# Optimization experiments

Measured on AMD Instinct MI355X. Metric: run time of the kernel, lower is better.

Reference implementation:

```python
import jax, jax.numpy as jnp
import numpy as np

D_MODEL = 2048
N_HEADS = 16
HEAD_DIM = D_MODEL // N_HEADS  # 128
HIDDEN = int(8 * D_MODEL / 3)  # 5461
EPS = 1e-6


def setup_inputs() -> dict:
    key = jax.random.key(0)
    ks = jax.random.split(key, 12)
    B, S = 2, 2048
    std = D_MODEL ** -0.5
    return {
        "x": jax.random.normal(ks[0], (B, S, D_MODEL), jnp.float32),
        "freq_cis": jax.random.normal(ks[1], (S, HEAD_DIM // 2, 2, 2), jnp.float32),
        "wq": jax.random.normal(ks[2], (D_MODEL, D_MODEL), jnp.float32) * std,
        "wk": jax.random.normal(ks[3], (D_MODEL, D_MODEL), jnp.float32) * std,
        "wv": jax.random.normal(ks[4], (D_MODEL, D_MODEL), jnp.float32) * std,
        "wo": jax.random.normal(ks[5], (D_MODEL, D_MODEL), jnp.float32) * std,
        "bo": jnp.zeros((D_MODEL,), jnp.float32),
        "w1": jax.random.normal(ks[6], (HIDDEN, D_MODEL), jnp.float32) * std,
        "w3": jax.random.normal(ks[7], (HIDDEN, D_MODEL), jnp.float32) * std,
        "w2": jax.random.normal(ks[8], (D_MODEL, HIDDEN), jnp.float32) * (HIDDEN ** -0.5),
        "g_attn": jnp.ones((D_MODEL,), jnp.float32),
        "g_ffn": jnp.ones((D_MODEL,), jnp.float32),
    }


def rmsnorm(x, g):
    xf = x.astype(jnp.float32)
    return xf * jax.lax.rsqrt(jnp.mean(xf * xf, axis=-1, keepdims=True) + EPS) * g


def rope(xq, xk, f):
    # xq/xk: [b, s, h, hd]; f: [s, hd/2, 2, 2]
    b, s, h, hd = xq.shape
    xq_ = xq.reshape(b, s, h, hd // 2, 2)
    xk_ = xk.reshape(b, s, h, hd // 2, 2)
    # out[b,s,h,i,j] = sum_k x[b,s,h,i,k] * f[s,i,j,k]
    q = jnp.einsum("bshik,sijk->bshij", xq_, f).reshape(b, s, h, hd)
    k = jnp.einsum("bshik,sijk->bshij", xk_, f).reshape(b, s, h, hd)
    return q, k


def reference(x, freq_cis, wq, wk, wv, wo, bo, w1, w3, w2, g_attn, g_ffn):
    b, s, d = x.shape
    h, hd = N_HEADS, HEAD_DIM
    scale = hd ** -0.5

    # --- attention sublayer ---
    xn = rmsnorm(x, g_attn)
    q = jnp.einsum("bsd,ed->bse", xn, wq).reshape(b, s, h, hd)
    k = jnp.einsum("bsd,ed->bse", xn, wk).reshape(b, s, h, hd)
    v = jnp.einsum("bsd,ed->bse", xn, wv).reshape(b, s, h, hd)
    q, k = rope(q, k, freq_cis[:s])
    attn = jnp.einsum("bqhd,bkhd->bhqk", q, k) * scale
    attn = jax.nn.softmax(attn, axis=-1)
    o = jnp.einsum("bhqk,bkhd->bqhd", attn, v).reshape(b, s, d)
    o = jnp.einsum("bsd,ed->bse", o, wo) + bo
    hres = x + o

    # --- SwiGLU FFN sublayer ---
    hn = rmsnorm(hres, g_ffn)
    x1 = jnp.einsum("bsd,hd->bsh", hn, w1)
    x3 = jnp.einsum("bsd,hd->bsh", hn, w3)
    ffn = jnp.einsum("bsh,dh->bsd", jax.nn.silu(x1) * x3, w2)
    return hres + ffn
```

## Files before the change

### kernel.cpp

```cpp
#include <hip/hip_runtime.h>

#define D_MODEL 2048
#define NHEADS 16
#define HDIM 128
#define HIDDEN_ 5461
#define HP2 5632
#define BATCH 2
#define SEQ 2048
#define MTOK 4096

typedef unsigned short u16;
typedef __attribute__((ext_vector_type(8))) short bf16x8;
typedef __attribute__((ext_vector_type(4))) float f32x4;

__device__ __forceinline__ u16 f2b(float f) {
  union { float f; unsigned u; } v; v.f = f;
  return (u16)((v.u + 0x7FFFu + ((v.u >> 16) & 1u)) >> 16);
}
__device__ __forceinline__ float b2f(u16 u) {
  union { unsigned u; float f; } v; v.u = ((unsigned)u) << 16;
  return v.f;
}
__device__ __forceinline__ void gload16(const void* g, void* l) {
  __builtin_amdgcn_global_load_lds(
      (const __attribute__((address_space(1))) unsigned int*)g,
      (__attribute__((address_space(3))) unsigned int*)l, 16, 0, 0);
}

#define SB0() __builtin_amdgcn_sched_barrier(0)
#define BARRIER() do { SB0(); __builtin_amdgcn_s_barrier(); SB0(); } while (0)
#define LGKM0() do { asm volatile("s_waitcnt lgkmcnt(0)" ::: "memory"); SB0(); } while (0)

__global__ __launch_bounds__(256) void k_conv8(const float* __restrict__ src,
                                               u16* __restrict__ dst, int n8) {
  int stride = gridDim.x * 256;
  for (int i = blockIdx.x * 256 + threadIdx.x; i < n8; i += stride) {
    const float4* s = (const float4*)src + (size_t)i * 2;
    float4 a = s[0], b = s[1];
    bf16x8 o;
    o[0] = f2b(a.x); o[1] = f2b(a.y); o[2] = f2b(a.z); o[3] = f2b(a.w);
    o[4] = f2b(b.x); o[5] = f2b(b.y); o[6] = f2b(b.z); o[7] = f2b(b.w);
    ((bf16x8*)dst)[i] = o;
  }
}

__global__ __launch_bounds__(256) void k_convpad(const float* __restrict__ src,
                                                 u16* __restrict__ dst,
                                                 int srows, int scols, int drows, int dcols) {
  size_t n = (size_t)drows * dcols;
  size_t stride = (size_t)gridDim.x * 256;
  for (size_t i = blockIdx.x * 256 + threadIdx.x; i < n; i += stride) {
    int r = (int)(i / dcols), c = (int)(i % dcols);
    float v = (r < srows && c < scols) ? src[(size_t)r * scols + c] : 0.f;
    dst[i] = f2b(v);
  }
}

__global__ __launch_bounds__(256) void k_rmsnorm(const float* __restrict__ X,
                                                 const float* __restrict__ G,
                                                 u16* __restrict__ Out) {
  int row = blockIdx.x;
  int tid = threadIdx.x;
  const float4* x4 = (const float4*)(X + (size_t)row * D_MODEL);
  float4 a = x4[tid * 2], b = x4[tid * 2 + 1];
  float ss = a.x * a.x + a.y * a.y + a.z * a.z + a.w * a.w +
             b.x * b.x + b.y * b.y + b.z * b.z + b.w * b.w;
#pragma unroll
  for (int off = 1; off < 64; off <<= 1) ss += __shfl_xor(ss, off);
  __shared__ float part[4];
  if ((tid & 63) == 0) part[tid >> 6] = ss;
  __syncthreads();
  float rstd = rsqrtf((part[0] + part[1] + part[2] + part[3]) * (1.0f / D_MODEL) + 1e-6f);
  const float4* g4 = (const float4*)G;
  float4 ga = g4[tid * 2], gb = g4[tid * 2 + 1];
  bf16x8 o;
  o[0] = f2b(a.x * rstd * ga.x); o[1] = f2b(a.y * rstd * ga.y);
  o[2] = f2b(a.z * rstd * ga.z); o[3] = f2b(a.w * rstd * ga.w);
  o[4] = f2b(b.x * rstd * gb.x); o[5] = f2b(b.y * rstd * gb.y);
  o[6] = f2b(b.z * rstd * gb.z); o[7] = f2b(b.w * rstd * gb.w);
  *((bf16x8*)(Out + (size_t)row * D_MODEL) + tid) = o;
}

template <int WN, int EPI>
__global__ __launch_bounds__(512, 2) void k_gemm2(const u16* __restrict__ A,
                                                  const u16* __restrict__ Bw,
                                                  void* __restrict__ O0,
                                                  void* __restrict__ O1,
                                                  void* __restrict__ O2,
                                                  const float* __restrict__ bias,
                                                  const float* __restrict__ res,
                                                  const u16* __restrict__ aux,
                                                  int M, int N, int K) {
  constexpr int BN = WN * 64;
  constexpr int PB = BN * 64;
  __shared__ __align__(128) char lds[65536 + 4 * PB];
  const int tid = threadIdx.x;
  const int w = tid >> 6, lane = tid & 63;
  const int lo = lane & 15, hi = lane >> 4;
  const int wr = w >> 2, wc = w & 3;

  const int ntN = N / BN;
  const int nwg = gridDim.x * gridDim.y;
  const int flat = blockIdx.y * gridDim.x + blockIdx.x;
  const int swz = (flat & 7) * (nwg >> 3) + (flat >> 3);
  const int tm = swz / ntN, tn = swz % ntN;
  const int m0 = tm * 256, n0 = tn * BN;

  auto stA = [&](int nb, int kk, int k0) {
#pragma unroll
    for (int j = 0; j < 2; ++j) {
      int row = j * 128 + (tid >> 2);
      const u16* g = A + (size_t)(m0 + row) * K + k0 + kk * 32 + (tid & 3) * 8;
      gload16(g, lds + nb * 32768 + kk * 16384 + j * 8192 + tid * 16);
    }
  };
  auto stB = [&](int nb, int kk, int k0) {
#pragma unroll
    for (int j = 0; j < WN / 2; ++j) {
      int row = j * 128 + (tid >> 2);
      const u16* g = Bw + (size_t)(n0 + row) * K + k0 + kk * 32 + (tid & 3) * 8;
      gload16(g, lds + 65536 + nb * 2 * PB + kk * PB + j * 8192 + tid * 16);
    }
  };
  auto ldA = [&](int buf, int kk, int mf) {
    return *(const bf16x8*)(lds + buf * 32768 + kk * 16384 +
                            (wr * 128 + mf * 16 + lo) * 64 + hi * 16);
  };
  auto ldB = [&](int buf, int kk, int nf) {
    return *(const bf16x8*)(lds + 65536 + buf * 2 * PB + kk * PB +
                            (wc * (WN * 16) + nf * 16 + lo) * 64 + hi * 16);
  };
#define VMCNT_CONFIRM()                                             \
  do {                                                              \
    if constexpr (WN == 4)                                          \
      asm volatile("s_waitcnt vmcnt(4)" ::: "memory");              \
    else                                                            \
      asm volatile("s_waitcnt vmcnt(3)" ::: "memory");              \
    SB0();                                                          \
  } while (0)

  f32x4 acc[8][WN];
#pragma unroll
  for (int i = 0; i < 8; i++)
#pragma unroll
    for (int j = 0; j < WN; j++) acc[i][j] = (f32x4){0.f, 0.f, 0.f, 0.f};

  stA(0, 0, 0);
  stB(0, 0, 0);
  stA(0, 1, 0);
  stB(0, 1, 0);
  VMCNT_CONFIRM();
  BARRIER();

  const int KT = K / 64;
  for (int kt = 0; kt < KT; ++kt) {
    const int buf = kt & 1, nb = buf ^ 1;
    int kn = (kt + 1) * 64;
    if (kn >= K) kn = 0;
    bf16x8 aF[4], bF[WN];

#pragma unroll
    for (int i = 0; i < 4; i++) aF[i] = ldA(buf, 0, i);
#pragma unroll
    for (int j = 0; j < WN; j++) bF[j] = ldB(buf, 0, j);
    stA(nb, 0, kn);
    BARRIER();
    LGKM0();
    __builtin_amdgcn_s_setprio(1);
#pragma unroll
    for (int i = 0; i < 4; i++)
#pragma unroll
      for (int j = 0; j < WN; j++)
        acc[i][j] = __builtin_amdgcn_mfma_f32_16x16x32_bf16(aF[i], bF[j], acc[i][j], 0, 0, 0);
    __builtin_amdgcn_s_setprio(0);
    BARRIER();

#pragma unroll
    for (int i = 0; i < 4; i++) aF[i] = ldA(buf, 0, 4 + i);
    stB(nb, 0, kn);
    VMCNT_CONFIRM();
    BARRIER();
    LGKM0();
    __builtin_amdgcn_s_setprio(1);
#pragma unroll
    for (int i = 0; i < 4; i++)
#pragma unroll
      for (int j = 0; j < WN; j++)
        acc[4 + i][j] = __builtin_amdgcn_mfma_f32_16x16x32_bf16(aF[i], bF[j], acc[4 + i][j], 0, 0, 0);
    __builtin_amdgcn_s_setprio(0);
    BARRIER();

#pragma unroll
    for (int i = 0; i < 4; i++) aF[i] = ldA(buf, 1, i);
#pragma unroll
    for (int j = 0; j < WN; j++) bF[j] = ldB(buf, 1, j);
    stA(nb, 1, kn);
    BARRIER();
    LGKM0();
    __builtin_amdgcn_s_setprio(1);
#pragma unroll
    for (int i = 0; i < 4; i++)
#pragma unroll
      for (int j = 0; j < WN; j++)
        acc[i][j] = __builtin_amdgcn_mfma_f32_16x16x32_bf16(aF[i], bF[j], acc[i][j], 0, 0, 0);
    __builtin_amdgcn_s_setprio(0);
    BARRIER();

#pragma unroll
    for (int i = 0; i < 4; i++) aF[i] = ldA(buf, 1, 4 + i);
    stB(nb, 1, kn);
    VMCNT_CONFIRM();
    BARRIER();
    LGKM0();
    __builtin_amdgcn_s_setprio(1);
#pragma unroll
    for (int i = 0; i < 4; i++)
#pragma unroll
      for (int j = 0; j < WN; j++)
        acc[4 + i][j] = __builtin_amdgcn_mfma_f32_16x16x32_bf16(aF[i], bF[j], acc[4 + i][j], 0, 0, 0);
    __builtin_amdgcn_s_setprio(0);
    BARRIER();
  }

  u16* qkvout = nullptr;
  int c0 = 0;
  if (EPI == 1) {
    int seg = n0 >> 11;
    qkvout = (u16*)(seg == 0 ? O0 : (seg == 1 ? O1 : O2));
    c0 = n0 & 2047;
  }
#pragma unroll
  for (int i = 0; i < 8; i++) {
#pragma unroll
    for (int j = 0; j < WN; j++) {
      int colL = wc * (WN * 16) + j * 16 + lo;
#pragma unroll
      for (int r = 0; r < 4; r++) {
        int row = m0 + wr * 128 + i * 16 + hi * 4 + r;
        float v = acc[i][j][r];
        if (EPI == 0) {
          ((u16*)O0)[(size_t)row * N + n0 + colL] = f2b(v);
        } else if (EPI == 1) {
          qkvout[(size_t)row * 2048 + c0 + colL] = f2b(v);
        } else if (EPI == 2) {
          size_t idx = (size_t)row * N + n0 + colL;
          ((float*)O0)[idx] = v + bias[n0 + colL] + res[idx];
        } else if (EPI == 3) {
          size_t idx = (size_t)row * N + n0 + colL;
          ((float*)O0)[idx] = v + res[idx];
        } else {
          size_t idx = (size_t)row * N + n0 + colL;
          float v1 = b2f(aux[idx]);
          float sig = 1.f / (1.f + __expf(-v1));
          ((u16*)O0)[idx] = f2b(v1 * sig * v);
        }
      }
    }
  }
#undef VMCNT_CONFIRM
}

__global__ __launch_bounds__(256) void k_rope(u16* __restrict__ Qb, u16* __restrict__ Kb,
                                              const float* __restrict__ F) {
  int n = MTOK * (D_MODEL / 2);
  int stride = gridDim.x * 256;
  for (int t = blockIdx.x * 256 + threadIdx.x; t < n; t += stride) {
    int i = t & 63;
    int rest = t >> 6;
    int hh = rest & 15;
    int tok = rest >> 4;
    int s = tok & (SEQ - 1);
    float4 f = ((const float4*)F)[s * 64 + i];
    size_t off = (size_t)tok * D_MODEL + hh * HDIM + i * 2;
    float x0 = b2f(Qb[off]), x1 = b2f(Qb[off + 1]);
    Qb[off] = f2b(x0 * f.x + x1 * f.y);
    Qb[off + 1] = f2b(x0 * f.z + x1 * f.w);
    x0 = b2f(Kb[off]); x1 = b2f(Kb[off + 1]);
    Kb[off] = f2b(x0 * f.x + x1 * f.y);
    Kb[off + 1] = f2b(x0 * f.z + x1 * f.w);
  }
}

__global__ __launch_bounds__(256) void k_vt(const u16* __restrict__ V, u16* __restrict__ VT) {
  __shared__ u16 t[64][72];
  const int stile = blockIdx.x;
  const int bh = blockIdx.y;
  const int dz = blockIdx.z;
  const int b = bh >> 4, h = bh & 15;
  const int tok0 = b * SEQ + stile * 64;
  const int d0 = dz * 64;
  const int tid = threadIdx.x;
#pragma unroll
  for (int p = 0; p < 2; p++) {
    int idx = p * 256 + tid;
    int row = idx >> 3, seg = idx & 7;
    bf16x8 v = *(const bf16x8*)(V + (size_t)(tok0 + row) * D_MODEL + h * HDIM + d0 + seg * 8);
    *(bf16x8*)(&t[row][seg * 8]) = v;
  }
  __syncthreads();
#pragma unroll
  for (int p = 0; p < 2; p++) {
    int idx = p * 256 + tid;
    int dr = idx >> 3, seg = idx & 7;
    bf16x8 o;
#pragma unroll
    for (int e = 0; e < 8; e++) o[e] = t[seg * 8 + e][dr];
    *(bf16x8*)(VT + ((size_t)bh * HDIM + d0 + dr) * SEQ + stile * 64 + seg * 8) = o;
  }
}

__global__ __launch_bounds__(256) void k_flash2(const u16* __restrict__ Q,
                                                const u16* __restrict__ Kb,
                                                const u16* __restrict__ VT,
                                                u16* __restrict__ O) {
  __shared__ u16 Kt[64 * 128];
  __shared__ u16 Vt[128 * 64];
  __shared__ u16 Pl[4][16 * 72];
  const int tid = threadIdx.x;
  const int w = tid >> 6, lane = tid & 63;
  const int lo = lane & 15, hi = lane >> 4;
  const int qt = blockIdx.x, bh = blockIdx.y;
  const int b = bh >> 4, h = bh & 15;
  const size_t qrow0 = (size_t)b * SEQ + qt * 64 + w * 16;
  const float SC = 0.08838834764831845f * 1.4426950408889634f;

  bf16x8 aQ[4];
#pragma unroll
  for (int kb = 0; kb < 4; kb++)
    aQ[kb] = *(const bf16x8*)(Q + (qrow0 + lo) * D_MODEL + h * HDIM + kb * 32 + hi * 8);

  float m_s[4], l_s[4];
  f32x4 oacc[8];
#pragma unroll
  for (int r = 0; r < 4; r++) { m_s[r] = -3.0e38f; l_s[r] = 0.f; }
#pragma unroll
  for (int d = 0; d < 8; d++) oacc[d] = (f32x4){0.f, 0.f, 0.f, 0.f};

  const int krowL = tid >> 4;
  const int kslot = (tid & 15) ^ (krowL & 7);
  const int vrowL = tid >> 3;
  const int vslot = (tid & 7) ^ (vrowL & 7);
  const u16* Kbase = Kb + (size_t)b * SEQ * D_MODEL + h * HDIM;
  const u16* Vbase = VT + (size_t)bh * HDIM * SEQ;

  for (int kt = 0; kt < SEQ / 64; kt++) {
    __syncthreads();
#pragma unroll
    for (int t = 0; t < 4; t++) {
      int row = t * 16 + krowL;
      const u16* g = Kbase + (size_t)(kt * 64 + row) * D_MODEL + kslot * 8;
      gload16(g, (char*)Kt + t * 4096 + tid * 16);
    }
#pragma unroll
    for (int t = 0; t < 4; t++) {
      int row = t * 32 + vrowL;
      const u16* g = Vbase + (size_t)row * SEQ + kt * 64 + vslot * 8;
      gload16(g, (char*)Vt + t * 4096 + tid * 16);
    }
    __syncthreads();

    f32x4 sf[4];
#pragma unroll
    for (int cb = 0; cb < 4; cb++) {
      f32x4 s = (f32x4){0.f, 0.f, 0.f, 0.f};
#pragma unroll
      for (int kb = 0; kb < 4; kb++) {
        int row = cb * 16 + lo;
        int ps = (kb * 4 + hi) ^ (lo & 7);
        bf16x8 bk = *(const bf16x8*)(Kt + row * 128 + ps * 8);
        s = __builtin_amdgcn_mfma_f32_16x16x32_bf16(aQ[kb], bk, s, 0, 0, 0);
      }
      sf[cb] = s;
    }

    float tm[4];
    bool okl = true;
#pragma unroll
    for (int r = 0; r < 4; r++) {
      float s0 = sf[0][r] * SC, s1 = sf[1][r] * SC;
      float s2 = sf[2][r] * SC, s3 = sf[3][r] * SC;
      sf[0][r] = s0; sf[1][r] = s1; sf[2][r] = s2; sf[3][r] = s3;
      float t = fmaxf(fmaxf(s0, s1), fmaxf(s2, s3));
#pragma unroll
      for (int off = 1; off < 16; off <<= 1) t = fmaxf(t, __shfl_xor(t, off));
      tm[r] = t;
      okl = okl && (t - m_s[r] <= 11.5f);
    }
    if (__all(okl)) {
#pragma unroll
      for (int r = 0; r < 4; r++) {
        float p0 = exp2f(sf[0][r] - m_s[r]), p1 = exp2f(sf[1][r] - m_s[r]);
        float p2 = exp2f(sf[2][r] - m_s[r]), p3 = exp2f(sf[3][r] - m_s[r]);
        float rs = (p0 + p1) + (p2 + p3);
#pragma unroll
        for (int off = 1; off < 16; off <<= 1) rs += __shfl_xor(rs, off);
        l_s[r] += rs;
        int prow = hi * 4 + r;
        Pl[w][prow * 72 + lo] = f2b(p0);
        Pl[w][prow * 72 + 16 + lo] = f2b(p1);
        Pl[w][prow * 72 + 32 + lo] = f2b(p2);
        Pl[w][prow * 72 + 48 + lo] = f2b(p3);
      }
    } else {
#pragma unroll
      for (int r = 0; r < 4; r++) {
        float mnew = fmaxf(m_s[r], tm[r]);
        float alpha = exp2f(m_s[r] - mnew);
        float p0 = exp2f(sf[0][r] - mnew), p1 = exp2f(sf[1][r] - mnew);
        float p2 = exp2f(sf[2][r] - mnew), p3 = exp2f(sf[3][r] - mnew);
        float rs = (p0 + p1) + (p2 + p3);
#pragma unroll
        for (int off = 1; off < 16; off <<= 1) rs += __shfl_xor(rs, off);
        l_s[r] = l_s[r] * alpha + rs;
        m_s[r] = mnew;
#pragma unroll
        for (int d = 0; d < 8; d++) oacc[d][r] *= alpha;
        int prow = hi * 4 + r;
        Pl[w][prow * 72 + lo] = f2b(p0);
        Pl[w][prow * 72 + 16 + lo] = f2b(p1);
        Pl[w][prow * 72 + 32 + lo] = f2b(p2);
        Pl[w][prow * 72 + 48 + lo] = f2b(p3);
      }
    }
    asm volatile("s_waitcnt lgkmcnt(0)" ::: "memory");
    bf16x8 aP[2];
#pragma unroll
    for (int ks = 0; ks < 2; ks++)
      aP[ks] = *(const bf16x8*)(&Pl[w][lo * 72 + ks * 32 + hi * 8]);
#pragma unroll
    for (int db = 0; db < 8; db++) {
#pragma unroll
      for (int ks = 0; ks < 2; ks++) {
        int row = db * 16 + lo;
        int ps = (ks * 4 + hi) ^ (lo & 7);
        bf16x8 bv = *(const bf16x8*)(Vt + row * 64 + ps * 8);
        oacc[db] = __builtin_amdgcn_mfma_f32_16x16x32_bf16(aP[ks], bv, oacc[db], 0, 0, 0);
      }
    }
  }
#pragma unroll
  for (int db = 0; db < 8; db++) {
#pragma unroll
    for (int r = 0; r < 4; r++) {
      size_t row = qrow0 + hi * 4 + r;
      float inv = 1.f / l_s[r];
      O[row * D_MODEL + h * HDIM + db * 16 + lo] = f2b(oacc[db][r] * inv);
    }
  }
}

extern "C" void kernel_launch(void* const* d_in, const int* in_sizes, int n_in,
                              void* d_out, int out_size, void* d_ws, size_t ws_size,
                              hipStream_t stream) {
  (void)in_sizes; (void)n_in; (void)out_size; (void)ws_size;
  const float* x  = (const float*)d_in[0];
  const float* fc = (const float*)d_in[1];
  const float* wq = (const float*)d_in[2];
  const float* wk = (const float*)d_in[3];
  const float* wv = (const float*)d_in[4];
  const float* wo = (const float*)d_in[5];
  const float* bo = (const float*)d_in[6];
  const float* w1 = (const float*)d_in[7];
  const float* w3 = (const float*)d_in[8];
  const float* w2 = (const float*)d_in[9];
  const float* ga = (const float*)d_in[10];
  const float* gf = (const float*)d_in[11];
  float* out = (float*)d_out;

  char* p = (char*)d_ws;
  auto alloc = [&](size_t bytes) { char* r = p; p += (bytes + 255) & ~(size_t)255; return r; };
  u16* xn  = (u16*)alloc((size_t)MTOK * D_MODEL * 2);
  u16* qb  = (u16*)alloc((size_t)MTOK * D_MODEL * 2);
  u16* kb  = (u16*)alloc((size_t)MTOK * D_MODEL * 2);
  u16* vb  = (u16*)alloc((size_t)MTOK * D_MODEL * 2);
  u16* x1  = (u16*)alloc((size_t)MTOK * HP2 * 2);
  u16* wsl = (u16*)alloc((size_t)3 * D_MODEL * D_MODEL * 2);
  u16* vbt = xn;
  u16* ob  = vb;
  u16* hn  = qb;

  k_rmsnorm<<<MTOK, 256, 0, stream>>>(x, ga, xn);
  k_conv8<<<1024, 256, 0, stream>>>(wq, wsl, D_MODEL * D_MODEL / 8);
  k_conv8<<<1024, 256, 0, stream>>>(wk, wsl + (size_t)D_MODEL * D_MODEL, D_MODEL * D_MODEL / 8);
  k_conv8<<<1024, 256, 0, stream>>>(wv, wsl + (size_t)2 * D_MODEL * D_MODEL, D_MODEL * D_MODEL / 8);
  k_gemm2<4, 1><<<dim3(6144 / 256, MTOK / 256), 512, 0, stream>>>(
      xn, wsl, qb, kb, vb, nullptr, nullptr, nullptr, MTOK, 6144, D_MODEL);
  k_rope<<<1024, 256, 0, stream>>>(qb, kb, fc);
  k_vt<<<dim3(SEQ / 64, BATCH * NHEADS, 2), 256, 0, stream>>>(vb, vbt);
  dim3 gfl(SEQ / 64, BATCH * NHEADS);
  k_flash2<<<gfl, 256, 0, stream>>>(qb, kb, vbt, ob);
  k_conv8<<<1024, 256, 0, stream>>>(wo, wsl, D_MODEL * D_MODEL / 8);
  k_gemm2<2, 2><<<dim3(2048 / 128, MTOK / 256), 512, 0, stream>>>(
      ob, wsl, out, nullptr, nullptr, bo, x, nullptr, MTOK, D_MODEL, D_MODEL);

  k_rmsnorm<<<MTOK, 256, 0, stream>>>(out, gf, hn);
  k_convpad<<<1024, 256, 0, stream>>>(w1, wsl, HIDDEN_, D_MODEL, HP2, D_MODEL);
  k_gemm2<4, 0><<<dim3(HP2 / 256, MTOK / 256), 512, 0, stream>>>(
      hn, wsl, x1, nullptr, nullptr, nullptr, nullptr, nullptr, MTOK, HP2, D_MODEL);
  k_convpad<<<1024, 256, 0, stream>>>(w3, wsl, HIDDEN_, D_MODEL, HP2, D_MODEL);
  k_gemm2<4, 4><<<dim3(HP2 / 256, MTOK / 256), 512, 0, stream>>>(
      hn, wsl, x1, nullptr, nullptr, nullptr, nullptr, x1, MTOK, HP2, D_MODEL);
  k_convpad<<<1024, 256, 0, stream>>>(w2, wsl, D_MODEL, HIDDEN_, D_MODEL, HP2);
  k_gemm2<2, 3><<<dim3(2048 / 128, MTOK / 256), 512, 0, stream>>>(
      x1, wsl, out, nullptr, nullptr, nullptr, out, nullptr, MTOK, D_MODEL, HP2);
}
```

Baseline: 852.8 us.

## Process two query tiles per wave in flash attention and retune GEMM tiles

The flash attention kernel now handles 128 query rows per block, two 16-row groups per wave. Each K and V fragment read from LDS is reused across both groups, and the MFMA operands are swapped to a transposed S/O layout. Softmax takes one max per column group with a packed bf16 convert, and the output store is vectorized. The three QKV weight conversions are merged into one launch, and several GEMMs switch to a narrower 128-column tile template. The cost is higher register pressure from doubled accumulators and more GEMM blocks.

Measured after the change: 819.3 us. 1.04x faster.

```diff
diff --git a/kernel.cpp b/kernel.cpp
--- a/kernel.cpp
+++ b/kernel.cpp
@@ -12,6 +12,7 @@
 typedef unsigned short u16;
 typedef __attribute__((ext_vector_type(8))) short bf16x8;
 typedef __attribute__((ext_vector_type(4))) float f32x4;
+typedef __attribute__((ext_vector_type(4))) short s16x4;
 
 __device__ __forceinline__ u16 f2b(float f) {
   union { float f; unsigned u; } v; v.f = f;
@@ -37,6 +38,25 @@
   for (int i = blockIdx.x * 256 + threadIdx.x; i < n8; i += stride) {
     const float4* s = (const float4*)src + (size_t)i * 2;
     float4 a = s[0], b = s[1];
+    bf16x8 o;
+    o[0] = f2b(a.x); o[1] = f2b(a.y); o[2] = f2b(a.z); o[3] = f2b(a.w);
+    o[4] = f2b(b.x); o[5] = f2b(b.y); o[6] = f2b(b.z); o[7] = f2b(b.w);
+    ((bf16x8*)dst)[i] = o;
+  }
+}
+
+__global__ __launch_bounds__(256) void k_conv3(const float* __restrict__ s0,
+                                               const float* __restrict__ s1,
+                                               const float* __restrict__ s2,
+                                               u16* __restrict__ dst) {
+  const int n8 = D_MODEL * D_MODEL / 8;
+  int total = 3 * n8;
+  int stride = gridDim.x * 256;
+  for (int i = blockIdx.x * 256 + threadIdx.x; i < total; i += stride) {
+    int seg = i >> 19, j = i & (n8 - 1);
+    const float* s = (seg == 0) ? s0 : (seg == 1 ? s1 : s2);
+    const float4* sp = (const float4*)s + (size_t)j * 2;
+    float4 a = sp[0], b = sp[1];
     bf16x8 o;
     o[0] = f2b(a.x); o[1] = f2b(a.y); o[2] = f2b(a.z); o[3] = f2b(a.w);
     o[4] = f2b(b.x); o[5] = f2b(b.y); o[6] = f2b(b.z); o[7] = f2b(b.w);
@@ -309,32 +329,34 @@
   }
 }
 
-__global__ __launch_bounds__(256) void k_flash2(const u16* __restrict__ Q,
+__global__ __launch_bounds__(256) void k_flash3(const u16* __restrict__ Q,
                                                 const u16* __restrict__ Kb,
                                                 const u16* __restrict__ VT,
                                                 u16* __restrict__ O) {
   __shared__ u16 Kt[64 * 128];
   __shared__ u16 Vt[128 * 64];
-  __shared__ u16 Pl[4][16 * 72];
+  __shared__ u16 Pl[4][2][16 * 72];
   const int tid = threadIdx.x;
   const int w = tid >> 6, lane = tid & 63;
   const int lo = lane & 15, hi = lane >> 4;
   const int qt = blockIdx.x, bh = blockIdx.y;
   const int b = bh >> 4, h = bh & 15;
-  const size_t qrow0 = (size_t)b * SEQ + qt * 64 + w * 16;
+  const size_t qrow0 = (size_t)b * SEQ + qt * 128 + w * 32;
   const float SC = 0.08838834764831845f * 1.4426950408889634f;
 
-  bf16x8 aQ[4];
-#pragma unroll
-  for (int kb = 0; kb < 4; kb++)
-    aQ[kb] = *(const bf16x8*)(Q + (qrow0 + lo) * D_MODEL + h * HDIM + kb * 32 + hi * 8);
-
-  float m_s[4], l_s[4];
-  f32x4 oacc[8];
-#pragma unroll
-  for (int r = 0; r < 4; r++) { m_s[r] = -3.0e38f; l_s[r] = 0.f; }
-#pragma unroll
-  for (int d = 0; d < 8; d++) oacc[d] = (f32x4){0.f, 0.f, 0.f, 0.f};
+  bf16x8 aQ[2][4];
+#pragma unroll
+  for (int qg = 0; qg < 2; qg++)
+#pragma unroll
+    for (int kb = 0; kb < 4; kb++)
+      aQ[qg][kb] = *(const bf16x8*)(Q + (qrow0 + qg * 16 + lo) * D_MODEL + h * HDIM + kb * 32 + hi * 8);
+
+  float m_s[2] = {-3.0e38f, -3.0e38f}, l_s[2] = {0.f, 0.f};
+  f32x4 oacc[2][8];
+#pragma unroll
+  for (int qg = 0; qg < 2; qg++)
+#pragma unroll
+    for (int d = 0; d < 8; d++) oacc[qg][d] = (f32x4){0.f, 0.f, 0.f, 0.f};
 
   const int krowL = tid >> 4;
   const int kslot = (tid & 15) ^ (krowL & 7);
@@ -342,6 +364,7 @@
   const int vslot = (tid & 7) ^ (vrowL & 7);
   const u16* Kbase = Kb + (size_t)b * SEQ * D_MODEL + h * HDIM;
   const u16* Vbase = VT + (size_t)bh * HDIM * SEQ;
+  unsigned* Plw = (unsigned*)&Pl[w][0][0];
 
   for (int kt = 0; kt < SEQ / 64; kt++) {
     __syncthreads();
@@ -359,92 +382,103 @@
     }
     __syncthreads();
 
-    f32x4 sf[4];
+    f32x4 sf[2][4];
 #pragma unroll
     for (int cb = 0; cb < 4; cb++) {
-      f32x4 s = (f32x4){0.f, 0.f, 0.f, 0.f};
+      bf16x8 kA[4];
 #pragma unroll
       for (int kb = 0; kb < 4; kb++) {
-        int row = cb * 16 + lo;
         int ps = (kb * 4 + hi) ^ (lo & 7);
-        bf16x8 bk = *(const bf16x8*)(Kt + row * 128 + ps * 8);
-        s = __builtin_amdgcn_mfma_f32_16x16x32_bf16(aQ[kb], bk, s, 0, 0, 0);
+        kA[kb] = *(const bf16x8*)(Kt + (cb * 16 + lo) * 128 + ps * 8);
       }
-      sf[cb] = s;
-    }
-
-    float tm[4];
-    bool okl = true;
-#pragma unroll
-    for (int r = 0; r < 4; r++) {
-      float s0 = sf[0][r] * SC, s1 = sf[1][r] * SC;
-      float s2 = sf[2][r] * SC, s3 = sf[3][r] * SC;
-      sf[0][r] = s0; sf[1][r] = s1; sf[2][r] = s2; sf[3][r] = s3;
-      float t = fmaxf(fmaxf(s0, s1), fmaxf(s2, s3));
-#pragma unroll
-      for (int off = 1; off < 16; off <<= 1) t = fmaxf(t, __shfl_xor(t, off));
-      tm[r] = t;
-      okl = okl && (t - m_s[r] <= 11.5f);
-    }
-    if (__all(okl)) {
-#pragma unroll
-      for (int r = 0; r < 4; r++) {
-        float p0 = exp2f(sf[0][r] - m_s[r]), p1 = exp2f(sf[1][r] - m_s[r]);
-        float p2 = exp2f(sf[2][r] - m_s[r]), p3 = exp2f(sf[3][r] - m_s[r]);
-        float rs = (p0 + p1) + (p2 + p3);
-#pragma unroll
-        for (int off = 1; off < 16; off <<= 1) rs += __shfl_xor(rs, off);
-        l_s[r] += rs;
-        int prow = hi * 4 + r;
-        Pl[w][prow * 72 + lo] = f2b(p0);
-        Pl[w][prow * 72 + 16 + lo] = f2b(p1);
-        Pl[w][prow * 72 + 32 + lo] = f2b(p2);
-        Pl[w][prow * 72 + 48 + lo] = f2b(p3);
+#pragma unroll
+      for (int qg = 0; qg < 2; qg++) {
+        f32x4 s = (f32x4){0.f, 0.f, 0.f, 0.f};
+#pragma unroll
+        for (int kb = 0; kb < 4; kb++)
+          s = __builtin_amdgcn_mfma_f32_16x16x32_bf16(kA[kb], aQ[qg][kb], s, 0, 0, 0);
+        sf[qg][cb] = s;
       }
-    } else {
-#pragma unroll
-      for (int r = 0; r < 4; r++) {
-        float mnew = fmaxf(m_s[r], tm[r]);
-        float alpha = exp2f(m_s[r] - mnew);
-        float p0 = exp2f(sf[0][r] - mnew), p1 = exp2f(sf[1][r] - mnew);
-        float p2 = exp2f(sf[2][r] - mnew), p3 = exp2f(sf[3][r] - mnew);
-        float rs = (p0 + p1) + (p2 + p3);
-#pragma unroll
-        for (int off = 1; off < 16; off <<= 1) rs += __shfl_xor(rs, off);
-        l_s[r] = l_s[r] * alpha + rs;
-        m_s[r] = mnew;
-#pragma unroll
-        for (int d = 0; d < 8; d++) oacc[d][r] *= alpha;
-        int prow = hi * 4 + r;
-        Pl[w][prow * 72 + lo] = f2b(p0);
-        Pl[w][prow * 72 + 16 + lo] = f2b(p1);
-        Pl[w][prow * 72 + 32 + lo] = f2b(p2);
-        Pl[w][prow * 72 + 48 + lo] = f2b(p3);
+    }
+
+    float tsc[2];
+    bool ok = true;
+#pragma unroll
+    for (int qg = 0; qg < 2; qg++) {
+      float t0 = fmaxf(fmaxf(sf[qg][0][0], sf[qg][0][1]), fmaxf(sf[qg][0][2], sf[qg][0][3]));
+      float t1 = fmaxf(fmaxf(sf[qg][1][0], sf[qg][1][1]), fmaxf(sf[qg][1][2], sf[qg][1][3]));
+      float t2 = fmaxf(fmaxf(sf[qg][2][0], sf[qg][2][1]), fmaxf(sf[qg][2][2], sf[qg][2][3]));
+      float t3 = fmaxf(fmaxf(sf[qg][3][0], sf[qg][3][1]), fmaxf(sf[qg][3][2], sf[qg][3][3]));
+      float t = fmaxf(fmaxf(t0, t1), fmaxf(t2, t3));
+      t = fmaxf(t, __shfl_xor(t, 16));
+      t = fmaxf(t, __shfl_xor(t, 32));
+      tsc[qg] = t * SC;
+      ok = ok && (tsc[qg] - m_s[qg] <= 11.5f);
+    }
+    bool skip = __all(ok);
+#pragma unroll
+    for (int qg = 0; qg < 2; qg++) {
+      float mm = m_s[qg];
+      if (!skip) {
+        mm = fmaxf(m_s[qg], tsc[qg]);
+        float alpha = exp2f(m_s[qg] - mm);
+        l_s[qg] *= alpha;
+#pragma unroll
+        for (int d = 0; d < 8; d++) oacc[qg][d] *= alpha;
+        m_s[qg] = mm;
       }
-    }
-    asm volatile("s_waitcnt lgkmcnt(0)" ::: "memory");
-    bf16x8 aP[2];
-#pragma unroll
-    for (int ks = 0; ks < 2; ks++)
-      aP[ks] = *(const bf16x8*)(&Pl[w][lo * 72 + ks * 32 + hi * 8]);
+      float rs = 0.f;
+#pragma unroll
+      for (int cb = 0; cb < 4; cb++) {
+        float p0 = exp2f(sf[qg][cb][0] * SC - mm);
+        float p1 = exp2f(sf[qg][cb][1] * SC - mm);
+        float p2 = exp2f(sf[qg][cb][2] * SC - mm);
+        float p3 = exp2f(sf[qg][cb][3] * SC - mm);
+        rs += (p0 + p1) + (p2 + p3);
+        unsigned pk0, pk1;
+        asm("v_cvt_pk_bf16_f32 %0, %1, %2" : "=v"(pk0) : "v"(p0), "v"(p1));
+        asm("v_cvt_pk_bf16_f32 %0, %1, %2" : "=v"(pk1) : "v"(p2), "v"(p3));
+        Plw[qg * 576 + lo * 36 + cb * 8 + hi * 2 + 0] = pk0;
+        Plw[qg * 576 + lo * 36 + cb * 8 + hi * 2 + 1] = pk1;
+      }
+      rs += __shfl_xor(rs, 16);
+      rs += __shfl_xor(rs, 32);
+      l_s[qg] += rs;
+    }
+    LGKM0();
+
+    bf16x8 aP[2][2];
+#pragma unroll
+    for (int qg = 0; qg < 2; qg++)
+#pragma unroll
+      for (int ks = 0; ks < 2; ks++)
+        aP[qg][ks] = *(const bf16x8*)(&Pl[w][qg][lo * 72 + ks * 32 + hi * 8]);
 #pragma unroll
     for (int db = 0; db < 8; db++) {
+      bf16x8 vA[2];
 #pragma unroll
       for (int ks = 0; ks < 2; ks++) {
-        int row = db * 16 + lo;
         int ps = (ks * 4 + hi) ^ (lo & 7);
-        bf16x8 bv = *(const bf16x8*)(Vt + row * 64 + ps * 8);
-        oacc[db] = __builtin_amdgcn_mfma_f32_16x16x32_bf16(aP[ks], bv, oacc[db], 0, 0, 0);
+        vA[ks] = *(const bf16x8*)(Vt + (db * 16 + lo) * 64 + ps * 8);
       }
-    }
-  }
-#pragma unroll
-  for (int db = 0; db < 8; db++) {
-#pragma unroll
-    for (int r = 0; r < 4; r++) {
-      size_t row = qrow0 + hi * 4 + r;
-      float inv = 1.f / l_s[r];
-      O[row * D_MODEL + h * HDIM + db * 16 + lo] = f2b(oacc[db][r] * inv);
+#pragma unroll
+      for (int qg = 0; qg < 2; qg++)
+#pragma unroll
+        for (int ks = 0; ks < 2; ks++)
+          oacc[qg][db] = __builtin_amdgcn_mfma_f32_16x16x32_bf16(vA[ks], aP[qg][ks], oacc[qg][db], 0, 0, 0);
+    }
+  }
+
+#pragma unroll
+  for (int qg = 0; qg < 2; qg++) {
+    float inv = 1.f / l_s[qg];
+    size_t rowoff = (qrow0 + qg * 16 + lo) * D_MODEL + h * HDIM;
+#pragma unroll
+    for (int db = 0; db < 8; db++) {
+      s16x4 o;
+#pragma unroll
+      for (int r = 0; r < 4; r++) o[r] = (short)f2b(oacc[qg][db][r] * inv);
+      *(s16x4*)(O + rowoff + db * 16 + hi * 4) = o;
     }
   }
 }
@@ -480,25 +514,23 @@
   u16* hn  = qb;
 
   k_rmsnorm<<<MTOK, 256, 0, stream>>>(x, ga, xn);
-  k_conv8<<<1024, 256, 0, stream>>>(wq, wsl, D_MODEL * D_MODEL / 8);
-  k_conv8<<<1024, 256, 0, stream>>>(wk, wsl + (size_t)D_MODEL * D_MODEL, D_MODEL * D_MODEL / 8);
-  k_conv8<<<1024, 256, 0, stream>>>(wv, wsl + (size_t)2 * D_MODEL * D_MODEL, D_MODEL * D_MODEL / 8);
-  k_gemm2<4, 1><<<dim3(6144 / 256, MTOK / 256), 512, 0, stream>>>(
+  k_conv3<<<1536, 256, 0, stream>>>(wq, wk, wv, wsl);
+  k_gemm2<2, 1><<<dim3(6144 / 128, MTOK / 256), 512, 0, stream>>>(
       xn, wsl, qb, kb, vb, nullptr, nullptr, nullptr, MTOK, 6144, D_MODEL);
   k_rope<<<1024, 256, 0, stream>>>(qb, kb, fc);
   k_vt<<<dim3(SEQ / 64, BATCH * NHEADS, 2), 256, 0, stream>>>(vb, vbt);
-  dim3 gfl(SEQ / 64, BATCH * NHEADS);
-  k_flash2<<<gfl, 256, 0, stream>>>(qb, kb, vbt, ob);
+  dim3 gfl(SEQ / 128, BATCH * NHEADS);
+  k_flash3<<<gfl, 256, 0, stream>>>(qb, kb, vbt, ob);
   k_conv8<<<1024, 256, 0, stream>>>(wo, wsl, D_MODEL * D_MODEL / 8);
   k_gemm2<2, 2><<<dim3(2048 / 128, MTOK / 256), 512, 0, stream>>>(
       ob, wsl, out, nullptr, nullptr, bo, x, nullptr, MTOK, D_MODEL, D_MODEL);
 
   k_rmsnorm<<<MTOK, 256, 0, stream>>>(out, gf, hn);
   k_convpad<<<1024, 256, 0, stream>>>(w1, wsl, HIDDEN_, D_MODEL, HP2, D_MODEL);
-  k_gemm2<4, 0><<<dim3(HP2 / 256, MTOK / 256), 512, 0, stream>>>(
+  k_gemm2<2, 0><<<dim3(HP2 / 128, MTOK / 256), 512, 0, stream>>>(
       hn, wsl, x1, nullptr, nullptr, nullptr, nullptr, nullptr, MTOK, HP2, D_MODEL);
   k_convpad<<<1024, 256, 0, stream>>>(w3, wsl, HIDDEN_, D_MODEL, HP2, D_MODEL);
-  k_gemm2<4, 4><<<dim3(HP2 / 256, MTOK / 256), 512, 0, stream>>>(
+  k_gemm2<2, 4><<<dim3(HP2 / 128, MTOK / 256), 512, 0, stream>>>(
       hn, wsl, x1, nullptr, nullptr, nullptr, nullptr, x1, MTOK, HP2, D_MODEL);
   k_convpad<<<1024, 256, 0, stream>>>(w2, wsl, D_MODEL, HIDDEN_, D_MODEL, HP2);
   k_gemm2<2, 3><<<dim3(2048 / 128, MTOK / 256), 512, 0, stream>>>(
```
